# Optimization experiments

Hardware: AMD Instinct MI355X
Metric: run time of the kernel (lower is better)

Reference implementation:

```python
import jax, jax.numpy as jnp
import numpy as np

DIM = 256
CDIM = 512
HEADS = 8
DIM_HEAD = 32
HID = HEADS * DIM_HEAD          # 256
MLP_DIM = int(DIM * 2.5)        # 640
B, T, TC = 8, 8192, 8192
GROUPS = 32
EPS = 1e-5


def setup_inputs() -> dict:
    key = jax.random.key(0)
    ks = jax.random.split(key, 12)
    w = lambda k, shape: jax.random.normal(k, shape, jnp.float32) * 0.02
    return {
        "x": jax.random.normal(ks[0], (B, DIM, T), jnp.float32),
        "c": jax.random.normal(ks[1], (B, CDIM, TC), jnp.float32),
        # self-attn (LinearAttention)
        "W_qkv": w(ks[2], (3 * HID, DIM)),
        "W_so": w(ks[3], (DIM, HID)), "b_so": jnp.zeros((DIM,), jnp.float32),
        "sa_g": jnp.ones((DIM,), jnp.float32), "sa_b": jnp.zeros((DIM,), jnp.float32),
        # cross-attn (LinearAttentionC)
        "W_cq": w(ks[4], (HID, DIM)),
        "W_ckv": w(ks[5], (2 * HID, CDIM)),
        "W_co": w(ks[6], (DIM, HID)), "b_co": jnp.zeros((DIM,), jnp.float32),
        "ca_g": jnp.ones((DIM,), jnp.float32), "ca_b": jnp.zeros((DIM,), jnp.float32),
        # MLP
        "W_m1": w(ks[7], (MLP_DIM, DIM)), "b_m1": jnp.zeros((MLP_DIM,), jnp.float32),
        "W_m2": w(ks[8], (DIM, MLP_DIM)), "b_m2": jnp.zeros((DIM,), jnp.float32),
        # pre-norms
        "nm_g": jnp.ones((DIM,), jnp.float32), "nm_b": jnp.zeros((DIM,), jnp.float32),
        "nm1_g": jnp.ones((DIM,), jnp.float32), "nm1_b": jnp.zeros((DIM,), jnp.float32),
        "nm2_g": jnp.ones((DIM,), jnp.float32), "nm2_b": jnp.zeros((DIM,), jnp.float32),
        "nm3_g": jnp.ones((CDIM,), jnp.float32), "nm3_b": jnp.zeros((CDIM,), jnp.float32),
    }


def group_norm(x, g, b):
    Bx, C, Tx = x.shape
    xg = x.reshape(Bx, GROUPS, C // GROUPS, Tx)
    mu = xg.mean(axis=(2, 3), keepdims=True)
    var = ((xg - mu) ** 2).mean(axis=(2, 3), keepdims=True)
    xn = ((xg - mu) * jax.lax.rsqrt(var + EPS)).reshape(Bx, C, Tx)
    return xn * g[None, :, None] + b[None, :, None]


def conv1(x, W, b=None):
    # 1x1 Conv1d == channel matmul: W [out, in], x [b, in, t]
    y = jnp.einsum('oc,bct->bot', W, x)
    return y if b is None else y + b[None, :, None]


def split_heads(t):
    Bx, HC, Tx = t.shape
    return t.reshape(Bx, HEADS, HC // HEADS, Tx)  # b h c t


def linear_attention(q, k, v):
    # q,k,v: [b, h, d, t]
    scale = DIM_HEAD ** -0.5
    q = jax.nn.softmax(q, axis=-2) * scale   # softmax over feature dim d
    k = jax.nn.softmax(k, axis=-1)           # softmax over time t
    ctx = jnp.einsum('bhdn,bhen->bhde', k, v)   # [b,h,d,e] tiny per-head context
    out = jnp.einsum('bhde,bhdn->bhen', ctx, q)
    Bx, H, E, Tx = out.shape
    return out.reshape(Bx, H * E, Tx)  # b (h c) t


def reference(x, c, W_qkv, W_so, b_so, sa_g, sa_b,
              W_cq, W_ckv, W_co, b_co, ca_g, ca_b,
              W_m1, b_m1, W_m2, b_m2,
              nm_g, nm_b, nm1_g, nm1_b, nm2_g, nm2_b, nm3_g, nm3_b):
    # --- self linear attention + residual ---
    h = group_norm(x, nm_g, nm_b)
    q, k, v = map(split_heads, jnp.split(conv1(h, W_qkv), 3, axis=1))
    o = linear_attention(q, k, v)
    o = group_norm(conv1(o, W_so, b_so), sa_g, sa_b)
    x = o + x
    # --- cross linear attention + residual ---
    h = group_norm(x, nm1_g, nm1_b)
    cn = group_norm(c, nm3_g, nm3_b)
    q = split_heads(conv1(h, W_cq))
    k, v = map(split_heads, jnp.split(conv1(cn, W_ckv), 2, axis=1))
    o = linear_attention(q, k, v)
    o = group_norm(conv1(o, W_co, b_co), ca_g, ca_b)
    x = o + x
    # --- SiLU MLP + residual ---
    h = group_norm(x, nm2_g, nm2_b)
    h = jax.nn.silu(conv1(h, W_m1, b_m1))
    x = conv1(h, W_m2, b_m2) + x
    return x
```

## Files before the change

kernel.cpp:

```cpp
#include <hip/hip_runtime.h>
#include <cmath>

typedef unsigned short u16;
typedef __attribute__((ext_vector_type(8))) __bf16 bf16x8;
typedef __attribute__((ext_vector_type(4))) float f32x4;

#define DEV static __device__ __forceinline__

DEV float b2f(u16 u){ union{unsigned i; float f;} v; v.i=((unsigned)u)<<16; return v.f; }
DEV u16 f2b(float f){ union{float f; unsigned i;} v; v.f=f; unsigned r = v.i + 0x7FFFu + ((v.i>>16)&1u); return (u16)(r>>16); }

#define GLL(g,l) __builtin_amdgcn_global_load_lds((const __attribute__((address_space(1))) void*)(g), (__attribute__((address_space(3))) void*)(l), 16, 0, 0)

__global__ void k_zero(float* p, int n){ int i = blockIdx.x*256+threadIdx.x; if(i<n) p[i]=0.f; }

__global__ void k_cvt3(const float* __restrict__ s0,const float* __restrict__ s1,
                       const float* __restrict__ s2, u16* __restrict__ d){
  int i = blockIdx.x*256 + threadIdx.x;
  if (i >= 294912) return;
  const float* s; int off;
  if      (i < 65536){ s=s0; off=0; }
  else if (i < 131072){ s=s1; off=65536; }
  else                { s=s2; off=131072; }
  d[i] = f2b(s[i-off]);
}

__global__ void k_fold(const float* __restrict__ W, const float* __restrict__ g,
                       const float* __restrict__ beta, const float* __restrict__ base,
                       const float* __restrict__ stats, u16* __restrict__ Wb,
                       float* __restrict__ biasb, int O, int K, int chsh, float inv_n){
  const int o = blockIdx.x, b = blockIdx.y;
  const int tid = threadIdx.x;
  float bp = 0.f;
  for (int k = tid; k < K; k += 256){
    const int gr = k >> chsh;
    const float s = stats[(b*32+gr)*2], s2 = stats[(b*32+gr)*2+1];
    const float mu = s*inv_n;
    const float rs = rsqrtf(s2*inv_n - mu*mu + 1e-5f);
    const float w = W[(long)o*K + k];
    const float gg = g[k]*rs;
    Wb[((long)b*O + o)*K + k] = f2b(w*gg);
    bp += w*(beta[k] - mu*gg);
  }
  __shared__ float red[256];
  red[tid] = bp; __syncthreads();
  for (int off=128; off>0; off>>=1){ if (tid<off) red[tid]+=red[tid+off]; __syncthreads(); }
  if (tid==0) biasb[b*O+o] = red[0] + (base ? base[o] : 0.f);
}

template<int CHSH>
__global__ void k_transs(const float* __restrict__ src, u16* __restrict__ dstRaw,
                         float* __restrict__ stat, int C){
  const int b = blockIdx.z;
  const int t0 = blockIdx.x*64, c0 = blockIdx.y*64;
  const int tid = threadIdx.x;
  __shared__ float tile[64][65];
  __shared__ float grp[16];
  if (tid < 16) grp[tid] = 0.f;
  float s_acc[4], s2_acc[4];
  #pragma unroll
  for (int p=0;p<4;p++){
    const int cc = (tid>>4) + p*16, tt = (tid&15)*4;
    const float4 v = *(const float4*)&src[((long)b*C + c0+cc)*8192 + t0+tt];
    tile[cc][tt+0]=v.x; tile[cc][tt+1]=v.y; tile[cc][tt+2]=v.z; tile[cc][tt+3]=v.w;
    s_acc[p]  = v.x+v.y+v.z+v.w;
    s2_acc[p] = v.x*v.x+v.y*v.y+v.z*v.z+v.w*v.w;
  }
  __syncthreads();
  #pragma unroll
  for (int p=0;p<4;p++){
    float s = s_acc[p], s2 = s2_acc[p];
    #pragma unroll
    for (int m=1; m<16; m<<=1){ s += __shfl_xor(s, m); s2 += __shfl_xor(s2, m); }
    if ((tid&15)==0){
      const int gl = ((tid>>4) + p*16) >> CHSH;
      atomicAdd(&grp[gl*2],   s);
      atomicAdd(&grp[gl*2+1], s2);
    }
  }
  #pragma unroll
  for (int p=0;p<4;p++){
    const int tt = (tid>>4) + p*16, c4 = (tid&15)*4;
    u16 rbi[4];
    #pragma unroll
    for (int j=0;j<4;j++) rbi[j] = f2b(tile[c4+j][tt]);
    ushort4 rv; rv.x=rbi[0]; rv.y=rbi[1]; rv.z=rbi[2]; rv.w=rbi[3];
    *(ushort4*)&dstRaw[((long)b*8192 + t0+tt)*C + c0+c4] = rv;
  }
  __syncthreads();
  const int ngr = 64>>CHSH;
  if (tid < ngr*2){
    atomicAdd(&stat[((b*32) + (c0>>CHSH))*2 + tid], grp[tid]);
  }
}

template<bool OUTB, bool BIAS, bool SILU, bool RES, bool STATS, bool SPLIT>
__global__ __launch_bounds__(256,2) void k_gemm(
    const u16* __restrict__ A, const u16* __restrict__ W,
    float* __restrict__ outF, u16* __restrict__ outB,
    const float* __restrict__ bias, const u16* __restrict__ res,
    float* __restrict__ stat, int K, int O, long wsb, int bsb)
{
  __shared__ u16 As[128*64];
  __shared__ u16 Ws[128*64];
  __shared__ float sb[128][2];
  const int tid = threadIdx.x;
  const int wv = tid>>6, lane = tid&63;
  const long t0 = (long)blockIdx.y*128;
  const int o0 = blockIdx.x*128;
  const int bb = (int)(t0>>13);
  const u16* Wp = W + (long)bb*wsb;
  const int wt = (wv>>1)*64, wo = (wv&1)*64;
  const int lr = lane>>3, lc = (lane&7)*8;
  f32x4 acc[4][4] = {};
  for (int kc = 0; kc < K; kc += 64){
    #pragma unroll
    for (int it = 0; it < 4; ++it){
      const int r = wv*32 + it*8;
      GLL(A + (t0 + r + lr)*(long)K + kc + lc, &As[r*64]);
      GLL(Wp + (long)(o0 + r + lr)*K + kc + lc, &Ws[r*64]);
    }
    __syncthreads();
    #pragma unroll
    for (int ks=0; ks<2; ++ks){
      const int kb = ks*32 + (lane>>4)*8;
      bf16x8 af[4], bfr[4];
      #pragma unroll
      for (int i=0;i<4;i++) af[i]  = *(const bf16x8*)&As[(wt + i*16 + (lane&15))*64 + kb];
      #pragma unroll
      for (int j=0;j<4;j++) bfr[j] = *(const bf16x8*)&Ws[(wo + j*16 + (lane&15))*64 + kb];
      #pragma unroll
      for (int i=0;i<4;i++)
        #pragma unroll
        for (int j=0;j<4;j++)
          acc[i][j] = __builtin_amdgcn_mfma_f32_16x16x32_bf16(af[i], bfr[j], acc[i][j], 0, 0, 0);
    }
    __syncthreads();
  }
  if (STATS){
    if (tid < 128){ sb[tid][0]=0.f; sb[tid][1]=0.f; }
    __syncthreads();
  }
  const int q = lane>>4, cc = lane&15;
  #pragma unroll
  for (int j=0;j<4;j++){
    const int o = o0 + wo + j*16 + cc;
    const float bv = BIAS ? bias[bsb*bb + o] : 0.f;
    float ts=0.f, ts2=0.f;
    #pragma unroll
    for (int i=0;i<4;i++){
      const long tb = t0 + wt + i*16 + q*4;
      #pragma unroll
      for (int r=0;r<4;r++){
        float v = acc[i][j][r] + bv;
        if (SILU) v = v * (1.f/(1.f + __expf(-v)));
        long idx;
        if (SPLIT) idx = ((long)(o>>8)<<24) + (tb + r)*256 + (o&255);
        else       idx = (tb + r)*(long)O + o;
        if (RES) v += b2f(res[idx]);
        if (STATS){ ts += v; ts2 += v*v; }
        if (OUTB) outB[idx] = f2b(v); else outF[idx] = v;
      }
    }
    if (STATS){
      const int ol = wo + j*16 + cc;
      atomicAdd(&sb[ol][0], ts);
      atomicAdd(&sb[ol][1], ts2);
    }
  }
  if (STATS){
    __syncthreads();
    if (tid < 16){
      float u=0.f, u2=0.f;
      #pragma unroll
      for (int j2=0;j2<8;j2++){ u += sb[tid*8+j2][0]; u2 += sb[tid*8+j2][1]; }
      atomicAdd(&stat[(bb*32 + (o0>>3) + tid)*2],   u);
      atomicAdd(&stat[(bb*32 + (o0>>3) + tid)*2+1], u2);
    }
  }
}

__global__ __launch_bounds__(256,2) void k_ctx(const u16* __restrict__ kp, const u16* __restrict__ vp,
                                               float* __restrict__ part){
  const int tid = threadIdx.x;
  const int b = blockIdx.x >> 6, seg = blockIdx.x & 63;
  const int h = tid>>5, d = tid&31;
  __shared__ u16 kb[16][256];
  __shared__ float vf[16][260];
  float acc[32];
  #pragma unroll
  for (int e=0;e<32;e++) acc[e]=0.f;
  float ks = 0.f;
  const long rb = (long)b*8192 + seg*128;
  const int w = tid>>6, sub = tid&63;
  for (int tc=0; tc<128; tc+=16){
    #pragma unroll
    for (int p=0;p<4;p++){
      const int row = p*4 + w;
      const long rowbase = (rb + tc + row)*256;
      if (sub < 32){
        uint4 val = *(const uint4*)(kp + rowbase + sub*8);
        *(uint4*)&kb[row][sub*8] = val;
      } else {
        const int s2 = sub-32;
        uint4 val = *(const uint4*)(vp + rowbase + s2*8);
        const u16* vs = (const u16*)&val;
        float4 f0 = {b2f(vs[0]),b2f(vs[1]),b2f(vs[2]),b2f(vs[3])};
        float4 f1 = {b2f(vs[4]),b2f(vs[5]),b2f(vs[6]),b2f(vs[7])};
        *(float4*)&vf[row][s2*8] = f0;
        *(float4*)&vf[row][s2*8+4] = f1;
      }
    }
    __syncthreads();
    #pragma unroll
    for (int r=0;r<16;r++){
      const float kpv = __expf(b2f(kb[r][h*32+d]));
      ks += kpv;
      #pragma unroll
      for (int e4=0;e4<8;e4++){
        const float4 v4 = *(const float4*)&vf[r][h*32+e4*4];
        acc[e4*4+0] += kpv*v4.x; acc[e4*4+1] += kpv*v4.y;
        acc[e4*4+2] += kpv*v4.z; acc[e4*4+3] += kpv*v4.w;
      }
    }
    __syncthreads();
  }
  float* pb = part + (long)blockIdx.x*8448;
  #pragma unroll
  for (int e=0;e<32;e++) pb[e*256 + tid] = acc[e];
  pb[8192 + tid] = ks;
}

__global__ void k_ctxred(const float* __restrict__ part, float* __restrict__ ctx,
                         float* __restrict__ ksumF){
  if (blockIdx.x >= 256){
    const int j = (blockIdx.x-256)*256 + threadIdx.x;
    #pragma unroll
    for (int q=0;q<4;q++){
      const int idx = j*4+q;
      const int b = idx>>8, cch = idx&255;
      float s=0.f;
      for (int g=0; g<64; g++) s += part[((long)(b*64+g))*8448 + 8192 + cch];
      ksumF[idx] = s;
    }
    return;
  }
  const int i = blockIdx.x*256 + threadIdx.x;
  const int b = i>>13, r = i&8191;
  float s=0.f;
  for (int g=0; g<64; g++) s += part[((long)(b*64+g))*8448 + r];
  ctx[i] = s;
}

__global__ void k_attnout(const u16* __restrict__ q, const float* __restrict__ ctx,
                          const float* __restrict__ ksumF, u16* __restrict__ out){
  const int b = blockIdx.x >> 8, t0 = (blockIdx.x & 255)*32;
  __shared__ float cs[8512];
  for (int i=threadIdx.x; i<8192; i+=256){
    const int e=i>>8, cch=i&255;
    cs[(cch>>5)*1064 + (cch&31)*33 + e] = ctx[(b<<13) + i] / ksumF[b*256 + cch];
  }
  __syncthreads();
  const int t = t0 + (threadIdx.x>>3), h = threadIdx.x&7;
  const u16* qp = q + ((long)b*8192 + t)*256 + h*32;
  uint4 qv[4];
  #pragma unroll
  for (int j=0;j<4;j++) qv[j] = ((const uint4*)qp)[j];
  const u16* qs = (const u16*)qv;
  float qe[32]; float ssum = 0.f;
  #pragma unroll
  for (int dd=0; dd<32; dd++){ qe[dd] = __expf(b2f(qs[dd])); ssum += qe[dd]; }
  const float inv = 0.17677669529663687f / ssum;
  float o[32];
  #pragma unroll
  for (int e=0;e<32;e++) o[e]=0.f;
  const float* ch = &cs[h*1064];
  #pragma unroll
  for (int dd=0; dd<32; dd++){
    const float w = qe[dd]*inv;
    #pragma unroll
    for (int e=0;e<32;e++) o[e] += w * ch[dd*33+e];
  }
  u16 ob[32];
  #pragma unroll
  for (int e=0;e<32;e++) ob[e] = f2b(o[e]);
  uint4* op = (uint4*)(out + ((long)b*8192 + t)*256 + h*32);
  const uint4* obv = (const uint4*)ob;
  #pragma unroll
  for (int j=0;j<4;j++) op[j] = obv[j];
}

__global__ void k_gnres(const u16* __restrict__ conv, u16* __restrict__ xr,
                        const float* __restrict__ sums_in, float* __restrict__ sums_out,
                        const float* __restrict__ g, const float* __restrict__ bt){
  const int blk = blockIdx.x;
  const int b = blk>>7;
  const long base = (long)blk*4096;
  const int tid = threadIdx.x;
  const int c0 = (tid<<2)&255;
  const int gr = c0>>3;
  const float s = sums_in[(b*32+gr)*2], s2 = sums_in[(b*32+gr)*2+1];
  const float mu = s*(1.f/65536.f);
  const float rs = rsqrtf(s2*(1.f/65536.f) - mu*mu + 1e-5f);
  float gg[4], bb[4];
  #pragma unroll
  for (int j=0;j<4;j++){ gg[j] = g[c0+j]*rs; bb[j] = bt[c0+j] - mu*gg[j]; }
  float ts=0.f, ts2=0.f;
  for (int it=0; it<16; ++it){
    const long i4 = base + it*256 + tid;
    ushort4 cv = ((const ushort4*)conv)[i4];
    ushort4 rv = ((const ushort4*)xr)[i4];
    float ov[4];
    const float ci[4] = {b2f(cv.x),b2f(cv.y),b2f(cv.z),b2f(cv.w)};
    const float ri[4] = {b2f(rv.x),b2f(rv.y),b2f(rv.z),b2f(rv.w)};
    #pragma unroll
    for (int j=0;j<4;j++){
      ov[j] = ci[j]*gg[j] + bb[j] + ri[j];
      ts += ov[j]; ts2 += ov[j]*ov[j];
    }
    ushort4 o4; o4.x=f2b(ov[0]); o4.y=f2b(ov[1]); o4.z=f2b(ov[2]); o4.w=f2b(ov[3]);
    ((ushort4*)xr)[i4] = o4;
  }
  __shared__ float grp[32][2];
  if (tid<32){ grp[tid][0]=0.f; grp[tid][1]=0.f; }
  __syncthreads();
  atomicAdd(&grp[gr][0], ts);
  atomicAdd(&grp[gr][1], ts2);
  __syncthreads();
  if (tid<32){
    atomicAdd(&sums_out[(b*32+tid)*2],   grp[tid][0]);
    atomicAdd(&sums_out[(b*32+tid)*2+1], grp[tid][1]);
  }
}

__global__ void k_final(const float* __restrict__ y, float* __restrict__ out){
  const int b = blockIdx.z;
  const int t0 = blockIdx.x*64, c0 = blockIdx.y*64;
  __shared__ float tile[64][65];
  #pragma unroll
  for (int p=0;p<4;p++){
    const int tt = (threadIdx.x>>4) + p*16, c4 = (threadIdx.x&15)*4;
    const float4 v = *(const float4*)&y[((long)b*8192 + t0+tt)*256 + c0+c4];
    tile[c4+0][tt]=v.x; tile[c4+1][tt]=v.y; tile[c4+2][tt]=v.z; tile[c4+3][tt]=v.w;
  }
  __syncthreads();
  #pragma unroll
  for (int p=0;p<4;p++){
    const int cc = (threadIdx.x>>4) + p*16, t4 = (threadIdx.x&15)*4;
    float4 v = {tile[cc][t4], tile[cc][t4+1], tile[cc][t4+2], tile[cc][t4+3]};
    *(float4*)&out[((long)b*256 + c0+cc)*8192 + t0+t4] = v;
  }
}

extern "C" void kernel_launch(void* const* d_in, const int* in_sizes, int n_in,
                              void* d_out, int out_size, void* d_ws, size_t ws_size,
                              hipStream_t stream){
  (void)in_sizes; (void)n_in; (void)out_size; (void)ws_size;
  const float* x   = (const float*)d_in[0];
  const float* c   = (const float*)d_in[1];
  const float* W_qkv=(const float*)d_in[2];
  const float* W_so =(const float*)d_in[3];
  const float* b_so =(const float*)d_in[4];
  const float* sa_g =(const float*)d_in[5];
  const float* sa_b =(const float*)d_in[6];
  const float* W_cq =(const float*)d_in[7];
  const float* W_ckv=(const float*)d_in[8];
  const float* W_co =(const float*)d_in[9];
  const float* b_co =(const float*)d_in[10];
  const float* ca_g =(const float*)d_in[11];
  const float* ca_b =(const float*)d_in[12];
  const float* W_m1 =(const float*)d_in[13];
  const float* b_m1 =(const float*)d_in[14];
  const float* W_m2 =(const float*)d_in[15];
  const float* b_m2 =(const float*)d_in[16];
  const float* nm_g =(const float*)d_in[17];
  const float* nm_b =(const float*)d_in[18];
  const float* nm1_g=(const float*)d_in[19];
  const float* nm1_b=(const float*)d_in[20];
  const float* nm2_g=(const float*)d_in[21];
  const float* nm2_b=(const float*)d_in[22];
  const float* nm3_g=(const float*)d_in[23];
  const float* nm3_b=(const float*)d_in[24];
  float* out = (float*)d_out;

  char* ws = (char*)d_ws;
  const size_t MB = 1024ull*1024ull;
  u16* wSO = (u16*)ws;
  u16* wCO = wSO + 65536;
  u16* wM2 = wCO + 65536;
  float* stats = (float*)(ws + 1*MB);
  float* xstat = stats;
  float* cstat = stats + 512;
  float* so_sum= stats + 1024;
  float* x1_sum= stats + 1536;
  float* co_sum= stats + 2048;
  float* x2_sum= stats + 2560;
  float* ksumF = stats + 3072;
  float* ctxb  = stats + 8192;
  float* bQKV = (float*)(ws + 2*MB);
  float* bCKV = bQKV + 6144;
  float* bCQ  = bCKV + 4096;
  float* bM1  = bCQ + 2048;
  u16* wQKVb = (u16*)(ws + 3*MB);
  u16* wCKVb = (u16*)(ws + 6*MB);
  u16* wCQb  = (u16*)(ws + 10*MB);
  u16* wM1b  = (u16*)(ws + 11*MB);
  u16*   xT    = (u16*)(ws + 16*MB);
  u16*   cT    = (u16*)(ws + 48*MB);
  float* part  = (float*)(ws + 112*MB);
  u16*   qkvb  = (u16*)(ws + 136*MB);
  u16*   kvb   = (u16*)(ws + 232*MB);
  u16*   convb = kvb;
  float* convF = (float*)kvb;
  u16*   attno = (u16*)(ws + 296*MB);
  const long SEG = 1L<<24;

  k_zero<<<12,256,0,stream>>>(stats, 3072);
  k_cvt3<<<1152,256,0,stream>>>(W_so, W_co, W_m2, wSO);

  k_transs<3><<<dim3(128,4,8),256,0,stream>>>(x, xT, xstat, 256);
  k_transs<4><<<dim3(128,8,8),256,0,stream>>>(c, cT, cstat, 512);

  k_fold<<<dim3(768,8),256,0,stream>>>(W_qkv, nm_g, nm_b, nullptr, xstat, wQKVb, bQKV, 768, 256, 3, 1.f/65536.f);
  k_fold<<<dim3(512,8),256,0,stream>>>(W_ckv, nm3_g, nm3_b, nullptr, cstat, wCKVb, bCKV, 512, 512, 4, 1.f/131072.f);
  k_gemm<true,true,false,false,false,true><<<dim3(6,512),256,0,stream>>>(xT, wQKVb, nullptr, qkvb, bQKV, nullptr, nullptr, 256, 768, 196608, 768);
  k_ctx<<<512,256,0,stream>>>(qkvb+SEG, qkvb+2*SEG, part);
  k_ctxred<<<258,256,0,stream>>>(part, ctxb, ksumF);
  k_attnout<<<2048,256,0,stream>>>(qkvb, ctxb, ksumF, attno);
  k_gemm<true,true,false,false,true,false><<<dim3(2,512),256,0,stream>>>(attno, wSO, nullptr, convb, b_so, nullptr, so_sum, 256, 256, 0, 0);
  k_gnres<<<1024,256,0,stream>>>(convb, xT, so_sum, x1_sum, sa_g, sa_b);

  k_fold<<<dim3(256,8),256,0,stream>>>(W_cq, nm1_g, nm1_b, nullptr, x1_sum, wCQb, bCQ, 256, 256, 3, 1.f/65536.f);
  k_gemm<true,true,false,false,false,false><<<dim3(2,512),256,0,stream>>>(xT, wCQb, nullptr, qkvb, bCQ, nullptr, nullptr, 256, 256, 65536, 256);
  k_gemm<true,true,false,false,false,true><<<dim3(4,512),256,0,stream>>>(cT, wCKVb, nullptr, kvb, bCKV, nullptr, nullptr, 512, 512, 262144, 512);
  k_ctx<<<512,256,0,stream>>>(kvb, kvb+SEG, part);
  k_ctxred<<<258,256,0,stream>>>(part, ctxb, ksumF);
  k_attnout<<<2048,256,0,stream>>>(qkvb, ctxb, ksumF, attno);
  k_gemm<true,true,false,false,true,false><<<dim3(2,512),256,0,stream>>>(attno, wCO, nullptr, convb, b_co, nullptr, co_sum, 256, 256, 0, 0);
  k_gnres<<<1024,256,0,stream>>>(convb, xT, co_sum, x2_sum, ca_g, ca_b);

  k_fold<<<dim3(640,8),256,0,stream>>>(W_m1, nm2_g, nm2_b, b_m1, x2_sum, wM1b, bM1, 640, 256, 3, 1.f/65536.f);
  k_gemm<true,true,true,false,false,false><<<dim3(5,512),256,0,stream>>>(xT, wM1b, nullptr, qkvb, bM1, nullptr, nullptr, 256, 640, 163840, 640);
  k_gemm<false,true,false,true,false,false><<<dim3(2,512),256,0,stream>>>(qkvb, wM2, convF, nullptr, b_m2, xT, nullptr, 640, 256, 0, 0);
  k_final<<<dim3(128,4,8),256,0,stream>>>(convF, out);
}
```

Before: 934.8 us.

## Merge setup kernels, remap GEMM workgroups, write final output transposed from GEMM

Several small launches are merged: zeroing and weight conversion become one init kernel, the two input transposes become one launch, and the first two weight folds share one launch. GEMM workgroups are remapped with a stride-8 permutation, likely to spread neighbouring tiles across XCDs for cache locality. The last MLP GEMM now writes fp32 output directly in [b,c,t] layout with float4 stores, which removes the separate k_final transpose pass and its intermediate buffer. The cost is strided output stores from the GEMM epilogue and extra runtime branching in the merged kernels.

```diff
diff --git a/kernel.cpp b/kernel.cpp
--- a/kernel.cpp
+++ b/kernel.cpp
@@ -12,12 +12,16 @@
 
 #define GLL(g,l) __builtin_amdgcn_global_load_lds((const __attribute__((address_space(1))) void*)(g), (__attribute__((address_space(3))) void*)(l), 16, 0, 0)
 
-__global__ void k_zero(float* p, int n){ int i = blockIdx.x*256+threadIdx.x; if(i<n) p[i]=0.f; }
-
-__global__ void k_cvt3(const float* __restrict__ s0,const float* __restrict__ s1,
-                       const float* __restrict__ s2, u16* __restrict__ d){
-  int i = blockIdx.x*256 + threadIdx.x;
-  if (i >= 294912) return;
+__global__ void k_init(const float* __restrict__ s0,const float* __restrict__ s1,
+                       const float* __restrict__ s2, u16* __restrict__ d,
+                       float* __restrict__ stats){
+  const int bid = blockIdx.x;
+  if (bid == 1152){
+    #pragma unroll
+    for (int j=0;j<12;j++){ const int idx=j*256+threadIdx.x; if (idx<3072) stats[idx]=0.f; }
+    return;
+  }
+  const int i = bid*256 + threadIdx.x;
   const float* s; int off;
   if      (i < 65536){ s=s0; off=0; }
   else if (i < 131072){ s=s1; off=65536; }
@@ -25,11 +29,9 @@
   d[i] = f2b(s[i-off]);
 }
 
-__global__ void k_fold(const float* __restrict__ W, const float* __restrict__ g,
-                       const float* __restrict__ beta, const float* __restrict__ base,
-                       const float* __restrict__ stats, u16* __restrict__ Wb,
-                       float* __restrict__ biasb, int O, int K, int chsh, float inv_n){
-  const int o = blockIdx.x, b = blockIdx.y;
+DEV void fold_body(const float* W, const float* g, const float* beta, const float* base,
+                   const float* stats, u16* Wb, float* biasb, int O, int K, int chsh,
+                   float inv_n, int o, int b){
   const int tid = threadIdx.x;
   float bp = 0.f;
   for (int k = tid; k < K; k += 256){
@@ -48,11 +50,33 @@
   if (tid==0) biasb[b*O+o] = red[0] + (base ? base[o] : 0.f);
 }
 
-template<int CHSH>
-__global__ void k_transs(const float* __restrict__ src, u16* __restrict__ dstRaw,
-                         float* __restrict__ stat, int C){
+__global__ void k_fold(const float* __restrict__ W, const float* __restrict__ g,
+                       const float* __restrict__ beta, const float* __restrict__ base,
+                       const float* __restrict__ stats, u16* __restrict__ Wb,
+                       float* __restrict__ biasb, int O, int K, int chsh, float inv_n){
+  fold_body(W,g,beta,base,stats,Wb,biasb,O,K,chsh,inv_n,blockIdx.x,blockIdx.y);
+}
+
+__global__ void k_fold2(const float* __restrict__ W1, const float* __restrict__ g1,
+                        const float* __restrict__ be1, const float* __restrict__ st1,
+                        u16* __restrict__ Wb1, float* __restrict__ bb1, int O1, int K1, int chsh1, float inv1,
+                        const float* __restrict__ W2, const float* __restrict__ g2,
+                        const float* __restrict__ be2, const float* __restrict__ st2,
+                        u16* __restrict__ Wb2, float* __restrict__ bb2, int O2, int K2, int chsh2, float inv2){
+  const int o = blockIdx.x, b = blockIdx.y;
+  if (o < O1) fold_body(W1,g1,be1,nullptr,st1,Wb1,bb1,O1,K1,chsh1,inv1,o,b);
+  else        fold_body(W2,g2,be2,nullptr,st2,Wb2,bb2,O2,K2,chsh2,inv2,o-O1,b);
+}
+
+__global__ void k_transs(const float* __restrict__ xsrc, const float* __restrict__ csrc,
+                         u16* __restrict__ xdst, u16* __restrict__ cdst,
+                         float* __restrict__ xstat, float* __restrict__ cstat){
   const int b = blockIdx.z;
-  const int t0 = blockIdx.x*64, c0 = blockIdx.y*64;
+  const int gy = blockIdx.y;
+  const float* src; u16* dst; float* stat; int C, chsh, c0;
+  if (gy < 4){ src=xsrc; dst=xdst; stat=xstat; C=256; chsh=3; c0=gy*64; }
+  else       { src=csrc; dst=cdst; stat=cstat; C=512; chsh=4; c0=(gy-4)*64; }
+  const int t0 = blockIdx.x*64;
   const int tid = threadIdx.x;
   __shared__ float tile[64][65];
   __shared__ float grp[16];
@@ -73,7 +97,7 @@
     #pragma unroll
     for (int m=1; m<16; m<<=1){ s += __shfl_xor(s, m); s2 += __shfl_xor(s2, m); }
     if ((tid&15)==0){
-      const int gl = ((tid>>4) + p*16) >> CHSH;
+      const int gl = ((tid>>4) + p*16) >> chsh;
       atomicAdd(&grp[gl*2],   s);
       atomicAdd(&grp[gl*2+1], s2);
     }
@@ -85,16 +109,16 @@
     #pragma unroll
     for (int j=0;j<4;j++) rbi[j] = f2b(tile[c4+j][tt]);
     ushort4 rv; rv.x=rbi[0]; rv.y=rbi[1]; rv.z=rbi[2]; rv.w=rbi[3];
-    *(ushort4*)&dstRaw[((long)b*8192 + t0+tt)*C + c0+c4] = rv;
+    *(ushort4*)&dst[((long)b*8192 + t0+tt)*C + c0+c4] = rv;
   }
   __syncthreads();
-  const int ngr = 64>>CHSH;
+  const int ngr = 64>>chsh;
   if (tid < ngr*2){
-    atomicAdd(&stat[((b*32) + (c0>>CHSH))*2 + tid], grp[tid]);
-  }
-}
-
-template<bool OUTB, bool BIAS, bool SILU, bool RES, bool STATS, bool SPLIT>
+    atomicAdd(&stat[((b*32) + (c0>>chsh))*2 + tid], grp[tid]);
+  }
+}
+
+template<bool OUTB, bool BIAS, bool SILU, bool RES, bool STATS, bool SPLIT, bool TRANS>
 __global__ __launch_bounds__(256,2) void k_gemm(
     const u16* __restrict__ A, const u16* __restrict__ W,
     float* __restrict__ outF, u16* __restrict__ outB,
@@ -106,8 +130,11 @@
   __shared__ float sb[128][2];
   const int tid = threadIdx.x;
   const int wv = tid>>6, lane = tid&63;
-  const long t0 = (long)blockIdx.y*128;
-  const int o0 = blockIdx.x*128;
+  const int nwg = (int)(gridDim.x*gridDim.y);
+  int fid = (int)(blockIdx.y*gridDim.x + blockIdx.x);
+  fid = (fid&7)*(nwg>>3) + (fid>>3);
+  const long t0 = (long)(fid / (int)gridDim.x)*128;
+  const int o0 = (fid % (int)gridDim.x)*128;
   const int bb = (int)(t0>>13);
   const u16* Wp = W + (long)bb*wsb;
   const int wt = (wv>>1)*64, wo = (wv&1)*64;
@@ -150,16 +177,29 @@
     #pragma unroll
     for (int i=0;i<4;i++){
       const long tb = t0 + wt + i*16 + q*4;
-      #pragma unroll
-      for (int r=0;r<4;r++){
-        float v = acc[i][j][r] + bv;
-        if (SILU) v = v * (1.f/(1.f + __expf(-v)));
-        long idx;
-        if (SPLIT) idx = ((long)(o>>8)<<24) + (tb + r)*256 + (o&255);
-        else       idx = (tb + r)*(long)O + o;
-        if (RES) v += b2f(res[idx]);
-        if (STATS){ ts += v; ts2 += v*v; }
-        if (OUTB) outB[idx] = f2b(v); else outF[idx] = v;
+      if (TRANS){
+        float vv[4];
+        #pragma unroll
+        for (int r=0;r<4;r++){
+          float v = acc[i][j][r] + bv;
+          if (SILU) v = v * (1.f/(1.f + __expf(-v)));
+          if (RES) v += b2f(res[(tb + r)*(long)O + o]);
+          vv[r] = v;
+        }
+        float4 v4; v4.x=vv[0]; v4.y=vv[1]; v4.z=vv[2]; v4.w=vv[3];
+        *(float4*)&outF[(((tb>>13)*(long)O + o)<<13) + (tb&8191)] = v4;
+      } else {
+        #pragma unroll
+        for (int r=0;r<4;r++){
+          float v = acc[i][j][r] + bv;
+          if (SILU) v = v * (1.f/(1.f + __expf(-v)));
+          long idx;
+          if (SPLIT) idx = ((long)(o>>8)<<24) + (tb + r)*256 + (o&255);
+          else       idx = (tb + r)*(long)O + o;
+          if (RES) v += b2f(res[idx]);
+          if (STATS){ ts += v; ts2 += v*v; }
+          if (OUTB) outB[idx] = f2b(v); else outF[idx] = v;
+        }
       }
     }
     if (STATS){
@@ -330,25 +370,6 @@
   if (tid<32){
     atomicAdd(&sums_out[(b*32+tid)*2],   grp[tid][0]);
     atomicAdd(&sums_out[(b*32+tid)*2+1], grp[tid][1]);
-  }
-}
-
-__global__ void k_final(const float* __restrict__ y, float* __restrict__ out){
-  const int b = blockIdx.z;
-  const int t0 = blockIdx.x*64, c0 = blockIdx.y*64;
-  __shared__ float tile[64][65];
-  #pragma unroll
-  for (int p=0;p<4;p++){
-    const int tt = (threadIdx.x>>4) + p*16, c4 = (threadIdx.x&15)*4;
-    const float4 v = *(const float4*)&y[((long)b*8192 + t0+tt)*256 + c0+c4];
-    tile[c4+0][tt]=v.x; tile[c4+1][tt]=v.y; tile[c4+2][tt]=v.z; tile[c4+3][tt]=v.w;
-  }
-  __syncthreads();
-  #pragma unroll
-  for (int p=0;p<4;p++){
-    const int cc = (threadIdx.x>>4) + p*16, t4 = (threadIdx.x&15)*4;
-    float4 v = {tile[cc][t4], tile[cc][t4+1], tile[cc][t4+2], tile[cc][t4+3]};
-    *(float4*)&out[((long)b*256 + c0+cc)*8192 + t0+t4] = v;
   }
 }
 
@@ -411,36 +432,32 @@
   u16*   qkvb  = (u16*)(ws + 136*MB);
   u16*   kvb   = (u16*)(ws + 232*MB);
   u16*   convb = kvb;
-  float* convF = (float*)kvb;
   u16*   attno = (u16*)(ws + 296*MB);
   const long SEG = 1L<<24;
 
-  k_zero<<<12,256,0,stream>>>(stats, 3072);
-  k_cvt3<<<1152,256,0,stream>>>(W_so, W_co, W_m2, wSO);
-
-  k_transs<3><<<dim3(128,4,8),256,0,stream>>>(x, xT, xstat, 256);
-  k_transs<4><<<dim3(128,8,8),256,0,stream>>>(c, cT, cstat, 512);
-
-  k_fold<<<dim3(768,8),256,0,stream>>>(W_qkv, nm_g, nm_b, nullptr, xstat, wQKVb, bQKV, 768, 256, 3, 1.f/65536.f);
-  k_fold<<<dim3(512,8),256,0,stream>>>(W_ckv, nm3_g, nm3_b, nullptr, cstat, wCKVb, bCKV, 512, 512, 4, 1.f/131072.f);
-  k_gemm<true,true,false,false,false,true><<<dim3(6,512),256,0,stream>>>(xT, wQKVb, nullptr, qkvb, bQKV, nullptr, nullptr, 256, 768, 196608, 768);
+  k_init<<<1153,256,0,stream>>>(W_so, W_co, W_m2, wSO, stats);
+
+  k_transs<<<dim3(128,12,8),256,0,stream>>>(x, c, xT, cT, xstat, cstat);
+
+  k_fold2<<<dim3(1280,8),256,0,stream>>>(W_qkv, nm_g, nm_b, xstat, wQKVb, bQKV, 768, 256, 3, 1.f/65536.f,
+                                         W_ckv, nm3_g, nm3_b, cstat, wCKVb, bCKV, 512, 512, 4, 1.f/131072.f);
+  k_gemm<true,true,false,false,false,true,false><<<dim3(6,512),256,0,stream>>>(xT, wQKVb, nullptr, qkvb, bQKV, nullptr, nullptr, 256, 768, 196608, 768);
   k_ctx<<<512,256,0,stream>>>(qkvb+SEG, qkvb+2*SEG, part);
   k_ctxred<<<258,256,0,stream>>>(part, ctxb, ksumF);
   k_attnout<<<2048,256,0,stream>>>(qkvb, ctxb, ksumF, attno);
-  k_gemm<true,true,false,false,true,false><<<dim3(2,512),256,0,stream>>>(attno, wSO, nullptr, convb, b_so, nullptr, so_sum, 256, 256, 0, 0);
+  k_gemm<true,true,false,false,true,false,false><<<dim3(2,512),256,0,stream>>>(attno, wSO, nullptr, convb, b_so, nullptr, so_sum, 256, 256, 0, 0);
   k_gnres<<<1024,256,0,stream>>>(convb, xT, so_sum, x1_sum, sa_g, sa_b);
 
   k_fold<<<dim3(256,8),256,0,stream>>>(W_cq, nm1_g, nm1_b, nullptr, x1_sum, wCQb, bCQ, 256, 256, 3, 1.f/65536.f);
-  k_gemm<true,true,false,false,false,false><<<dim3(2,512),256,0,stream>>>(xT, wCQb, nullptr, qkvb, bCQ, nullptr, nullptr, 256, 256, 65536, 256);
-  k_gemm<true,true,false,false,false,true><<<dim3(4,512),256,0,stream>>>(cT, wCKVb, nullptr, kvb, bCKV, nullptr, nullptr, 512, 512, 262144, 512);
+  k_gemm<true,true,false,false,false,false,false><<<dim3(2,512),256,0,stream>>>(xT, wCQb, nullptr, qkvb, bCQ, nullptr, nullptr, 256, 256, 65536, 256);
+  k_gemm<true,true,false,false,false,true,false><<<dim3(4,512),256,0,stream>>>(cT, wCKVb, nullptr, kvb, bCKV, nullptr, nullptr, 512, 512, 262144, 512);
   k_ctx<<<512,256,0,stream>>>(kvb, kvb+SEG, part);
   k_ctxred<<<258,256,0,stream>>>(part, ctxb, ksumF);
   k_attnout<<<2048,256,0,stream>>>(qkvb, ctxb, ksumF, attno);
-  k_gemm<true,true,false,false,true,false><<<dim3(2,512),256,0,stream>>>(attno, wCO, nullptr, convb, b_co, nullptr, co_sum, 256, 256, 0, 0);
+  k_gemm<true,true,false,false,true,false,false><<<dim3(2,512),256,0,stream>>>(attno, wCO, nullptr, convb, b_co, nullptr, co_sum, 256, 256, 0, 0);
   k_gnres<<<1024,256,0,stream>>>(convb, xT, co_sum, x2_sum, ca_g, ca_b);
 
   k_fold<<<dim3(640,8),256,0,stream>>>(W_m1, nm2_g, nm2_b, b_m1, x2_sum, wM1b, bM1, 640, 256, 3, 1.f/65536.f);
-  k_gemm<true,true,true,false,false,false><<<dim3(5,512),256,0,stream>>>(xT, wM1b, nullptr, qkvb, bM1, nullptr, nullptr, 256, 640, 163840, 640);
-  k_gemm<false,true,false,true,false,false><<<dim3(2,512),256,0,stream>>>(qkvb, wM2, convF, nullptr, b_m2, xT, nullptr, 640, 256, 0, 0);
-  k_final<<<dim3(128,4,8),256,0,stream>>>(convF, out);
-}
+  k_gemm<true,true,true,false,false,false,false><<<dim3(5,512),256,0,stream>>>(xT, wM1b, nullptr, qkvb, bM1, nullptr, nullptr, 256, 640, 163840, 640);
+  k_gemm<false,true,false,true,false,false,true><<<dim3(2,512),256,0,stream>>>(qkvb, wM2, out, nullptr, b_m2, xT, nullptr, 640, 256, 0, 0);
+}
```

Result: faster. 873.4 us (-6.6%).
